# Kernel optimization log

Measured on AMD Instinct MI355X. Metric: run time of the kernel, lower is better.

Reference implementation:

```python
import jax, jax.numpy as jnp
import numpy as np

N = 50000      # nodes
E = 600000     # edges (no self-loops in data; GATConv adds them)
IN = 128       # input_dim
HID = 16       # hidden_dim
H1 = 8         # heads1
H2 = 4         # heads2
OUT = 40       # output_dim (classes)
EPS_BN = 1e-5
NEG_SLOPE = 0.2


def setup_inputs() -> dict:
    key = jax.random.key(0)
    ks = jax.random.split(key, 40)
    f32 = jnp.float32

    def p(k, shape, scale=0.1):
        return (jax.random.normal(k, shape) * scale).astype(f32)

    x = jax.random.normal(ks[0], (N, IN), f32)
    src = jax.random.randint(ks[1], (E,), 0, N)
    off = jax.random.randint(ks[2], (E,), 1, N)
    dst = (src + off) % N  # guarantees src != dst
    edge_index = jnp.stack([src, dst]).astype(jnp.int32)

    D1 = HID * H1  # 128
    D2 = HID * H2  # 64
    inp = {
        "x": x, "edge_index": edge_index,
        # conv1: IN -> HID per head, H1 heads, concat
        "W1": p(ks[3], (IN, H1 * HID)), "as1": p(ks[4], (H1, HID)), "ad1": p(ks[5], (H1, HID)), "b1": p(ks[6], (D1,)),
        "g1": jnp.ones((D1,), f32), "be1": jnp.zeros((D1,), f32),
        # conv_mid: D1 -> D1, 1 head, mean (concat=False)
        "Wm": p(ks[7], (D1, D1)), "asm": p(ks[8], (1, D1)), "adm": p(ks[9], (1, D1)), "bm": p(ks[10], (D1,)),
        "gm": jnp.ones((D1,), f32), "bem": jnp.zeros((D1,), f32),
        # conv2: D1 -> HID per head, H2 heads, concat
        "W2": p(ks[11], (D1, H2 * HID)), "as2": p(ks[12], (H2, HID)), "ad2": p(ks[13], (H2, HID)), "b2": p(ks[14], (D2,)),
        "g2": jnp.ones((D2,), f32), "be2": jnp.zeros((D2,), f32),
        # conv3: D2 -> OUT, 1 head, mean
        "W3": p(ks[15], (D2, OUT)), "as3": p(ks[16], (1, OUT)), "ad3": p(ks[17], (1, OUT)), "b3": p(ks[18], (OUT,)),
        "g3": jnp.ones((OUT,), f32), "be3": jnp.zeros((OUT,), f32),
    }
    return inp


def _gat(x, src, dst, W, a_s, a_d, b, concat):
    """PyG GATConv forward (self-loops already appended to src/dst)."""
    Nn = x.shape[0]
    H, C = a_s.shape
    h = (x @ W).reshape(Nn, H, C)                       # [N,H,C]
    s = (h * a_s).sum(-1)                               # [N,H] source score
    d = (h * a_d).sum(-1)                               # [N,H] dest score
    e = jax.nn.leaky_relu(s[src] + d[dst], NEG_SLOPE)   # [E,H]
    # segment softmax over incoming edges of each dst node
    m = jax.ops.segment_max(e, dst, num_segments=Nn)    # [N,H]
    ee = jnp.exp(e - m[dst])
    den = jax.ops.segment_sum(ee, dst, num_segments=Nn)
    alpha = ee / (den[dst] + 1e-16)                     # [E,H]
    out = jax.ops.segment_sum(h[src] * alpha[:, :, None], dst, num_segments=Nn)  # [N,H,C]
    out = out.reshape(Nn, H * C) if concat else out.mean(axis=1)
    return out + b


def _bn(x, g, b):
    mu = x.mean(axis=0)
    var = x.var(axis=0)
    return g * (x - mu) * jax.lax.rsqrt(var + EPS_BN) + b


def reference(x, edge_index, W1, as1, ad1, b1, g1, be1, Wm, asm, adm, bm, gm, bem,
              W2, as2, ad2, b2, g2, be2, W3, as3, ad3, b3, g3, be3):
    Nn = x.shape[0]
    loops = jnp.arange(Nn, dtype=edge_index.dtype)
    src = jnp.concatenate([edge_index[0], loops])
    dst = jnp.concatenate([edge_index[1], loops])

    h = jax.nn.elu(_bn(_gat(x, src, dst, W1, as1, ad1, b1, True), g1, be1))
    res = h
    h = jax.nn.elu(_bn(_gat(h, src, dst, Wm, asm, adm, bm, False), gm, bem))
    h = res + h
    h = jax.nn.elu(_bn(_gat(h, src, dst, W2, as2, ad2, b2, True), g2, be2))
    h = _bn(_gat(h, src, dst, W3, as3, ad3, b3, False), g3, be3)
    return jax.nn.log_softmax(h, axis=1)
```

## Files before the change

### kernel.cpp

```cpp
#include <hip/hip_runtime.h>
#include <hip/hip_bf16.h>
#include <math.h>

#define NN 50000
#define NE 600000
#define ET (NN + NE)

typedef __hip_bfloat16 bf16;
typedef __attribute__((ext_vector_type(8))) short bf16x8;
typedef __attribute__((ext_vector_type(4))) float f32x4;

static __device__ inline unsigned short f2bf(float f) {
    union { __hip_bfloat16 h; unsigned short u; } v;
    v.h = __float2bfloat16(f);
    return v.u;
}
static __device__ inline float bf2f(bf16 h) { return __bfloat162float(h); }

__global__ void k_hist(const int* __restrict__ ei, int* __restrict__ deg) {
    int e = blockIdx.x * blockDim.x + threadIdx.x;
    if (e >= ET) return;
    int d = (e < NE) ? ei[NE + e] : (e - NE);
    atomicAdd(&deg[d], 1);
}

__global__ void k_scan_local(const int* __restrict__ deg, int* __restrict__ tmp,
                             int* __restrict__ csum) {
    __shared__ int wsum[16];
    int i = blockIdx.x * 1024 + threadIdx.x;
    int lane = threadIdx.x & 63, wid = threadIdx.x >> 6;
    int x = (i < NN) ? deg[i] : 0;
    for (int off = 1; off < 64; off <<= 1) {
        int y = __shfl_up(x, off);
        if (lane >= off) x += y;
    }
    if (lane == 63) wsum[wid] = x;
    __syncthreads();
    if (wid == 0) {
        int t = (lane < 16) ? wsum[lane] : 0;
        for (int off = 1; off < 16; off <<= 1) {
            int y = __shfl_up(t, off);
            if (lane >= off) t += y;
        }
        if (lane < 16) wsum[lane] = t;
    }
    __syncthreads();
    if (wid > 0) x += wsum[wid - 1];
    if (i < NN) tmp[i] = x;
    if (threadIdx.x == 1023) csum[blockIdx.x] = x;
}

__global__ void k_scan_chunks(int* __restrict__ csum, int nchunks) {
    int lane = threadIdx.x;
    int v = (lane < nchunks) ? csum[lane] : 0;
    for (int off = 1; off < 64; off <<= 1) {
        int y = __shfl_up(v, off);
        if (lane >= off) v += y;
    }
    if (lane < nchunks) csum[lane] = v;
}

__global__ void k_rowptr(const int* __restrict__ tmp, const int* __restrict__ csum,
                         int* __restrict__ rowptr) {
    int i = blockIdx.x * blockDim.x + threadIdx.x;
    if (i == 0) rowptr[0] = 0;
    if (i < NN) {
        int chunk = i >> 10;
        int off = (chunk > 0) ? csum[chunk - 1] : 0;
        rowptr[i + 1] = tmp[i] + off;
    }
}

__global__ void k_fill(const int* __restrict__ ei, const int* __restrict__ rowptr,
                       int* __restrict__ fill, int* __restrict__ csr) {
    int e = blockIdx.x * blockDim.x + threadIdx.x;
    if (e >= ET) return;
    int s = (e < NE) ? ei[e] : (e - NE);
    int d = (e < NE) ? ei[NE + e] : (e - NE);
    int pos = atomicAdd(&fill[d], 1);
    csr[rowptr[d] + pos] = s;
}

__global__ void k_wconv_all(const float* __restrict__ W1, const float* __restrict__ Wm,
                            const float* __restrict__ W2, short* __restrict__ WT1,
                            short* __restrict__ WTm, short* __restrict__ WT2) {
    int idx = blockIdx.x * 256 + threadIdx.x;
    if (idx < 16384) {
        int d = idx >> 7, k = idx & 127;
        WT1[idx] = (short)f2bf(W1[k * 128 + d]);
    } else if (idx < 32768) {
        int i2 = idx - 16384;
        int d = i2 >> 7, k = i2 & 127;
        WTm[i2] = (short)f2bf(Wm[k * 128 + d]);
    } else if (idx < 40960) {
        int i3 = idx - 32768;
        int d = i3 >> 7, k = i3 & 127;
        WT2[i3] = (short)f2bf(W2[k * 64 + d]);
    }
}

template <int D>
__global__ void k_bnfin(const float* __restrict__ sums, const float* __restrict__ g,
                        const float* __restrict__ be, float2* __restrict__ ss) {
    int c = threadIdx.x;
    if (c >= D) return;
    float mu = sums[c] * (1.f / NN);
    float var = sums[128 + c] * (1.f / NN) - mu * mu;
    float sc = g[c] * rsqrtf(var + 1e-5f);
    ss[c] = make_float2(sc, be[c] - mu * sc);
}

template <int D, int HF, int MODE>
__global__ __launch_bounds__(64) void k_gemm_mfma(const float* __restrict__ Xf,
                                                  const bf16* __restrict__ X1,
                                                  const float2* __restrict__ ss1,
                                                  const bf16* __restrict__ X2,
                                                  const float2* __restrict__ ss2,
                                                  const short* __restrict__ WT,
                                                  bf16* __restrict__ Hout,
                                                  const float* __restrict__ a_s,
                                                  const float* __restrict__ a_d,
                                                  float* __restrict__ S,
                                                  float* __restrict__ Dv) {
    constexpr int K = 128;
    constexpr int NT = D / 16;
    int lane = threadIdx.x;
    int rb = blockIdx.x * 16;
    int m = lane & 15, kg = lane >> 4;

    f32x4 acc[NT];
#pragma unroll
    for (int n = 0; n < NT; n++) acc[n] = (f32x4){0.f, 0.f, 0.f, 0.f};

#pragma unroll
    for (int k0 = 0; k0 < K; k0 += 32) {
        int cb = k0 + kg * 8;
        bf16x8 a;
        if constexpr (MODE == 0) {
            const float* xp = Xf + (size_t)(rb + m) * K + cb;
            float4 f0 = *reinterpret_cast<const float4*>(xp);
            float4 f1 = *reinterpret_cast<const float4*>(xp + 4);
            a[0] = (short)f2bf(f0.x); a[1] = (short)f2bf(f0.y);
            a[2] = (short)f2bf(f0.z); a[3] = (short)f2bf(f0.w);
            a[4] = (short)f2bf(f1.x); a[5] = (short)f2bf(f1.y);
            a[6] = (short)f2bf(f1.z); a[7] = (short)f2bf(f1.w);
        } else {
            bf16x8 r1 = *reinterpret_cast<const bf16x8*>(X1 + (size_t)(rb + m) * K + cb);
            bf16x8 r2;
            if constexpr (MODE == 2)
                r2 = *reinterpret_cast<const bf16x8*>(X2 + (size_t)(rb + m) * K + cb);
#pragma unroll
            for (int j = 0; j < 8; j++) {
                float2 p1 = ss1[cb + j];
                bf16 b1; *(short*)&b1 = r1[j];
                float v = p1.x * bf2f(b1) + p1.y;
                v = (v > 0.f) ? v : (__expf(v) - 1.f);
                if constexpr (MODE == 2) {
                    float2 p2 = ss2[cb + j];
                    bf16 b2; *(short*)&b2 = r2[j];
                    float v2 = p2.x * bf2f(b2) + p2.y;
                    v2 = (v2 > 0.f) ? v2 : (__expf(v2) - 1.f);
                    v += v2;
                }
                a[j] = (short)f2bf(v);
            }
        }
#pragma unroll
        for (int n = 0; n < NT; n++) {
            bf16x8 b = *reinterpret_cast<const bf16x8*>(WT + (size_t)(n * 16 + m) * K + cb);
            acc[n] = __builtin_amdgcn_mfma_f32_16x16x32_bf16(a, b, acc[n], 0, 0, 0);
        }
    }

    float asv[NT], adv[NT];
#pragma unroll
    for (int n = 0; n < NT; n++) {
        asv[n] = a_s[n * 16 + m];
        adv[n] = a_d[n * 16 + m];
    }
#pragma unroll
    for (int r = 0; r < 4; r++) {
        int row = rb + kg * 4 + r;
#pragma unroll
        for (int n = 0; n < NT; n++)
            Hout[(size_t)row * D + n * 16 + m] = __float2bfloat16(acc[n][r]);
        if constexpr (HF == 1) {
            float sa = 0.f, da = 0.f;
#pragma unroll
            for (int n = 0; n < NT; n++) {
                sa += acc[n][r] * asv[n];
                da += acc[n][r] * adv[n];
            }
            for (int off = 1; off < 16; off <<= 1) {
                sa += __shfl_xor(sa, off);
                da += __shfl_xor(da, off);
            }
            if (m == 0) { S[row] = sa; Dv[row] = da; }
        } else {
#pragma unroll
            for (int n = 0; n < NT; n++) {
                float sa = acc[n][r] * asv[n];
                float da = acc[n][r] * adv[n];
                for (int off = 1; off < 16; off <<= 1) {
                    sa += __shfl_xor(sa, off);
                    da += __shfl_xor(da, off);
                }
                if (m == 0) { S[row * HF + n] = sa; Dv[row * HF + n] = da; }
            }
        }
    }
}

__global__ void k_gemm_small(const bf16* __restrict__ X, const float2* __restrict__ ss,
                             const float* __restrict__ W, bf16* __restrict__ Hout,
                             const float* __restrict__ a_s, const float* __restrict__ a_d,
                             float* __restrict__ S, float* __restrict__ Dv) {
    __shared__ float xs[64];
    int n = blockIdx.x, t = threadIdx.x;
    {
        float2 p = ss[t];
        float v = p.x * bf2f(X[n * 64 + t]) + p.y;
        xs[t] = (v > 0.f) ? v : (__expf(v) - 1.f);
    }
    __syncthreads();
    float acc = 0.f;
    if (t < 40) {
#pragma unroll
        for (int k = 0; k < 64; k++) acc += xs[k] * W[k * 40 + t];
        Hout[n * 40 + t] = __float2bfloat16(acc);
    }
    float sa = (t < 40) ? acc * a_s[t] : 0.f;
    float da = (t < 40) ? acc * a_d[t] : 0.f;
    for (int off = 32; off; off >>= 1) {
        sa += __shfl_xor(sa, off);
        da += __shfl_xor(da, off);
    }
    if (t == 0) {
        S[n] = sa;
        Dv[n] = da;
    }
}

template <int H, int C, int D>
__global__ __launch_bounds__(256) void k_aggregate(const bf16* __restrict__ Hb,
                                                   const float* __restrict__ S,
                                                   const float* __restrict__ Dv,
                                                   const int* __restrict__ rowptr,
                                                   const int* __restrict__ csr,
                                                   bf16* __restrict__ Out) {
    constexpr int WCAP = 64;
    __shared__ float wl[4][WCAP * H];
    int nl = threadIdx.x >> 6;
    int node = blockIdx.x * 4 + nl;
    if (node >= NN) return;
    int lane = threadIdx.x & 63;
    int r0 = rowptr[node], r1 = rowptr[node + 1];
    int cnt = r1 - r0;
    float dn[H], den[H];
#pragma unroll
    for (int h = 0; h < H; h++) {
        dn[h] = Dv[node * H + h];
        den[h] = 0.f;
    }
    for (int k = lane; k < cnt; k += 64) {
        int u = csr[r0 + k];
        float sv[H];
        if constexpr (H == 8) {
            float4 s0 = *reinterpret_cast<const float4*>(S + (size_t)u * 8);
            float4 s1 = *reinterpret_cast<const float4*>(S + (size_t)u * 8 + 4);
            sv[0] = s0.x; sv[1] = s0.y; sv[2] = s0.z; sv[3] = s0.w;
            sv[4] = s1.x; sv[5] = s1.y; sv[6] = s1.z; sv[7] = s1.w;
        } else if constexpr (H == 4) {
            float4 s0 = *reinterpret_cast<const float4*>(S + (size_t)u * 4);
            sv[0] = s0.x; sv[1] = s0.y; sv[2] = s0.z; sv[3] = s0.w;
        } else {
            sv[0] = S[u];
        }
        float ex[H];
#pragma unroll
        for (int h = 0; h < H; h++) {
            float e = sv[h] + dn[h];
            e = fmaxf(e, 0.2f * e);
            ex[h] = __expf(e);
            den[h] += ex[h];
        }
        if (k < WCAP) {
#pragma unroll
            for (int h = 0; h < H; h++) wl[nl][k * H + h] = ex[h];
        }
    }
#pragma unroll
    for (int h = 0; h < H; h++) {
        for (int off = 32; off; off >>= 1) den[h] += __shfl_xor(den[h], off);
        den[h] = 1.f / (den[h] + 1e-16f);
    }

    constexpr int EPI = (D > 64) ? 1 : 2;
    constexpr int LP = 64 / EPI;
    int sub = lane / LP;
    int j = lane % LP;
    bool act = (2 * j) < D;
    const int h_l = act ? (2 * j) / C : 0;
    float dninv_l = den[0], dn_l = dn[0];
#pragma unroll
    for (int h = 1; h < H; h++) {
        dninv_l = (h_l == h) ? den[h] : dninv_l;
        dn_l = (h_l == h) ? dn[h] : dn_l;
    }
    const float* wlp = &wl[nl][0];
    auto wof = [&](int idx, int u) -> float {
        if (idx < WCAP) return wlp[idx * H + h_l];
        float e = S[(size_t)u * H + h_l] + dn_l;
        e = fmaxf(e, 0.2f * e);
        return __expf(e);
    };
    float ax = 0.f, ay = 0.f;
    int k = sub;
    for (; k + 3 * EPI < cnt; k += 4 * EPI) {
        int u0 = csr[r0 + k];
        int u1 = csr[r0 + k + EPI];
        int u2 = csr[r0 + k + 2 * EPI];
        int u3 = csr[r0 + k + 3 * EPI];
        unsigned p0 = 0, p1 = 0, p2 = 0, p3 = 0;
        if (act) {
            p0 = *reinterpret_cast<const unsigned*>(Hb + (size_t)u0 * D + 2 * j);
            p1 = *reinterpret_cast<const unsigned*>(Hb + (size_t)u1 * D + 2 * j);
            p2 = *reinterpret_cast<const unsigned*>(Hb + (size_t)u2 * D + 2 * j);
            p3 = *reinterpret_cast<const unsigned*>(Hb + (size_t)u3 * D + 2 * j);
        }
        float w0 = wof(k, u0), w1 = wof(k + EPI, u1);
        float w2 = wof(k + 2 * EPI, u2), w3 = wof(k + 3 * EPI, u3);
        ax += w0 * __uint_as_float(p0 << 16) + w1 * __uint_as_float(p1 << 16) +
              w2 * __uint_as_float(p2 << 16) + w3 * __uint_as_float(p3 << 16);
        ay += w0 * __uint_as_float(p0 & 0xffff0000u) + w1 * __uint_as_float(p1 & 0xffff0000u) +
              w2 * __uint_as_float(p2 & 0xffff0000u) + w3 * __uint_as_float(p3 & 0xffff0000u);
    }
    for (; k < cnt; k += EPI) {
        int u = csr[r0 + k];
        unsigned pv = 0;
        if (act) pv = *reinterpret_cast<const unsigned*>(Hb + (size_t)u * D + 2 * j);
        float w = wof(k, u);
        ax += w * __uint_as_float(pv << 16);
        ay += w * __uint_as_float(pv & 0xffff0000u);
    }
    if (EPI == 2) {
        ax += __shfl_xor(ax, 32);
        ay += __shfl_xor(ay, 32);
    }
    if (act && lane < LP) {
        unsigned o = (unsigned)f2bf(ax * dninv_l) | ((unsigned)f2bf(ay * dninv_l) << 16);
        *reinterpret_cast<unsigned*>(Out + (size_t)node * D + 2 * j) = o;
    }
}

template <int D>
__global__ void k_bnstats(const bf16* __restrict__ X, float* __restrict__ sums) {
    int col = threadIdx.x;
    if (col >= D) return;
    float s = 0.f, q = 0.f;
    for (int r = blockIdx.x; r < NN; r += gridDim.x) {
        float v = bf2f(X[(size_t)r * D + col]);
        s += v;
        q += v * v;
    }
    atomicAdd(&sums[col], s);
    atomicAdd(&sums[128 + col], q);
}

__global__ void k_bn_logsoftmax(const bf16* __restrict__ X, const float* __restrict__ sums,
                                const float* __restrict__ g, const float* __restrict__ be,
                                float* __restrict__ Out) {
    int node = (blockIdx.x * blockDim.x + threadIdx.x) >> 6;
    int lane = threadIdx.x & 63;
    if (node >= NN) return;
    float bnv = 0.f, v = -1e30f;
    if (lane < 40) {
        float mu = sums[lane] * (1.f / NN);
        float var = sums[128 + lane] * (1.f / NN) - mu * mu;
        float sc = g[lane] * rsqrtf(var + 1e-5f);
        bnv = sc * (bf2f(X[node * 40 + lane]) - mu) + be[lane];
        v = bnv;
    }
    float m = v;
    for (int off = 32; off; off >>= 1) m = fmaxf(m, __shfl_xor(m, off));
    float ex = (lane < 40) ? expf(bnv - m) : 0.f;
    for (int off = 32; off; off >>= 1) ex += __shfl_xor(ex, off);
    float lse = m + logf(ex);
    if (lane < 40) Out[node * 40 + lane] = bnv - lse;
}

extern "C" void kernel_launch(void* const* d_in, const int* in_sizes, int n_in,
                              void* d_out, int out_size, void* d_ws, size_t ws_size,
                              hipStream_t stream) {
    (void)in_sizes; (void)n_in; (void)out_size; (void)ws_size;
    const float* x   = (const float*)d_in[0];
    const int*   ei  = (const int*)d_in[1];
    const float* W1  = (const float*)d_in[2];
    const float* as1 = (const float*)d_in[3];
    const float* ad1 = (const float*)d_in[4];
    const float* g1  = (const float*)d_in[6];
    const float* be1 = (const float*)d_in[7];
    const float* Wm  = (const float*)d_in[8];
    const float* asm_ = (const float*)d_in[9];
    const float* adm = (const float*)d_in[10];
    const float* gm  = (const float*)d_in[12];
    const float* bem = (const float*)d_in[13];
    const float* W2  = (const float*)d_in[14];
    const float* as2 = (const float*)d_in[15];
    const float* ad2 = (const float*)d_in[16];
    const float* g2  = (const float*)d_in[18];
    const float* be2 = (const float*)d_in[19];
    const float* W3  = (const float*)d_in[20];
    const float* as3 = (const float*)d_in[21];
    const float* ad3 = (const float*)d_in[22];
    const float* g3  = (const float*)d_in[24];
    const float* be3 = (const float*)d_in[25];
    float* out = (float*)d_out;

    char* ws = (char*)d_ws;
    size_t off = 0;
    auto alloc = [&](size_t b) {
        void* p = ws + off;
        off = (off + b + 255) & ~(size_t)255;
        return p;
    };
    int* rowptr = (int*)alloc((NN + 1) * 4);
    int* csr    = (int*)alloc((size_t)ET * 4);
    int* deg    = (int*)alloc(NN * 4);
    int* tmp    = (int*)alloc(NN * 4);
    int* csum   = (int*)alloc(256 * 4);
    bf16* Hbf   = (bf16*)alloc((size_t)NN * 128 * 2);
    bf16* AG1   = (bf16*)alloc((size_t)NN * 128 * 2);
    bf16* AG2   = (bf16*)alloc((size_t)NN * 128 * 2);
    bf16* AG3   = (bf16*)alloc((size_t)NN * 64 * 2);
    bf16* AG4   = (bf16*)alloc((size_t)NN * 40 * 2);
    float* S    = (float*)alloc((size_t)NN * 8 * 4);
    float* Dv   = (float*)alloc((size_t)NN * 8 * 4);
    float* bns  = (float*)alloc(4 * 256 * 4);
    float2* ss1 = (float2*)alloc(128 * 8);
    float2* ssM = (float2*)alloc(128 * 8);
    float2* ss2 = (float2*)alloc(64 * 8);
    short* WT1  = (short*)alloc(128 * 128 * 2);
    short* WTm  = (short*)alloc(128 * 128 * 2);
    short* WT2  = (short*)alloc(128 * 64 * 2);

    const int nchunks = (NN + 1023) / 1024;

    hipMemsetAsync(bns, 0, 4 * 256 * 4, stream);
    k_wconv_all<<<160, 256, 0, stream>>>(W1, Wm, W2, WT1, WTm, WT2);

    hipMemsetAsync(deg, 0, NN * 4, stream);
    k_hist<<<(ET + 255) / 256, 256, 0, stream>>>(ei, deg);
    k_scan_local<<<nchunks, 1024, 0, stream>>>(deg, tmp, csum);
    k_scan_chunks<<<1, 64, 0, stream>>>(csum, nchunks);
    k_rowptr<<<(NN + 255) / 256, 256, 0, stream>>>(tmp, csum, rowptr);
    hipMemsetAsync(deg, 0, NN * 4, stream);
    k_fill<<<(ET + 255) / 256, 256, 0, stream>>>(ei, rowptr, deg, csr);

    const int mfma_blocks = NN / 16;
    const int node_wave_blocks = (NN + 3) / 4;

    k_gemm_mfma<128, 8, 0><<<mfma_blocks, 64, 0, stream>>>(x, nullptr, nullptr, nullptr, nullptr,
                                                           WT1, Hbf, as1, ad1, S, Dv);
    k_aggregate<8, 16, 128><<<node_wave_blocks, 256, 0, stream>>>(Hbf, S, Dv, rowptr, csr, AG1);
    k_bnstats<128><<<512, 128, 0, stream>>>(AG1, bns + 0 * 256);
    k_bnfin<128><<<1, 128, 0, stream>>>(bns + 0 * 256, g1, be1, ss1);

    k_gemm_mfma<128, 1, 1><<<mfma_blocks, 64, 0, stream>>>(nullptr, AG1, ss1, nullptr, nullptr,
                                                           WTm, Hbf, asm_, adm, S, Dv);
    k_aggregate<1, 128, 128><<<node_wave_blocks, 256, 0, stream>>>(Hbf, S, Dv, rowptr, csr, AG2);
    k_bnstats<128><<<512, 128, 0, stream>>>(AG2, bns + 1 * 256);
    k_bnfin<128><<<1, 128, 0, stream>>>(bns + 1 * 256, gm, bem, ssM);

    k_gemm_mfma<64, 4, 2><<<mfma_blocks, 64, 0, stream>>>(nullptr, AG2, ssM, AG1, ss1,
                                                          WT2, Hbf, as2, ad2, S, Dv);
    k_aggregate<4, 16, 64><<<node_wave_blocks, 256, 0, stream>>>(Hbf, S, Dv, rowptr, csr, AG3);
    k_bnstats<64><<<512, 64, 0, stream>>>(AG3, bns + 2 * 256);
    k_bnfin<64><<<1, 64, 0, stream>>>(bns + 2 * 256, g2, be2, ss2);

    k_gemm_small<<<NN, 64, 0, stream>>>(AG3, ss2, W3, Hbf, as3, ad3, S, Dv);
    k_aggregate<1, 40, 40><<<node_wave_blocks, 256, 0, stream>>>(Hbf, S, Dv, rowptr, csr, AG4);
    k_bnstats<40><<<512, 64, 0, stream>>>(AG4, bns + 3 * 256);
    k_bn_logsoftmax<<<node_wave_blocks, 256, 0, stream>>>(AG4, bns + 3 * 256, g3, be3, out);
}
```

Before: 581.0 us.

## Fuse setup kernels, merge BN finalize into stats, simplify aggregate softmax

Merges the histogram with the weight conversion, the chunk scan with rowptr, and the CSR fill with the first-layer GEMM into single launches. BN finalize is folded into the stats kernel through a last-block counter. The three memsets become one. The aggregate kernel drops its separate denominator pass and LDS weight cache and computes the softmax denominator inline with the weighted sum, using batched loads. Together these cut launch count and a pass over edge scores, at the cost of recomputing exp per lane group and adding atomic and fence overhead in the BN finalize.

New measurement: 565.1 us. 2.7% less time.

```diff
diff --git a/kernel.cpp b/kernel.cpp
--- a/kernel.cpp
+++ b/kernel.cpp
@@ -5,6 +5,9 @@
 #define NN 50000
 #define NE 600000
 #define ET (NN + NE)
+#define FILLB ((ET + 255) / 256)
+#define NTILE (NN / 16)
+#define GEMMB ((NTILE + 3) / 4)
 
 typedef __hip_bfloat16 bf16;
 typedef __attribute__((ext_vector_type(8))) short bf16x8;
@@ -17,11 +20,32 @@
 }
 static __device__ inline float bf2f(bf16 h) { return __bfloat162float(h); }
 
-__global__ void k_hist(const int* __restrict__ ei, int* __restrict__ deg) {
-    int e = blockIdx.x * blockDim.x + threadIdx.x;
-    if (e >= ET) return;
-    int d = (e < NE) ? ei[NE + e] : (e - NE);
-    atomicAdd(&deg[d], 1);
+__global__ void k_hist_wconv(const int* __restrict__ ei, int* __restrict__ deg,
+                             const float* __restrict__ W1, const float* __restrict__ Wm,
+                             const float* __restrict__ W2, short* __restrict__ WT1,
+                             short* __restrict__ WTm, short* __restrict__ WT2) {
+    int b = blockIdx.x;
+    if (b < FILLB) {
+        int e = b * 256 + threadIdx.x;
+        if (e < ET) {
+            int d = (e < NE) ? ei[NE + e] : (e - NE);
+            atomicAdd(&deg[d], 1);
+        }
+    } else {
+        int idx = (b - FILLB) * 256 + threadIdx.x;
+        if (idx < 16384) {
+            int d = idx >> 7, k = idx & 127;
+            WT1[idx] = (short)f2bf(W1[k * 128 + d]);
+        } else if (idx < 32768) {
+            int i2 = idx - 16384;
+            int d = i2 >> 7, k = i2 & 127;
+            WTm[i2] = (short)f2bf(Wm[k * 128 + d]);
+        } else if (idx < 40960) {
+            int i3 = idx - 32768;
+            int d = i3 >> 7, k = i3 & 127;
+            WT2[i3] = (short)f2bf(W2[k * 64 + d]);
+        }
+    }
 }
 
 __global__ void k_scan_local(const int* __restrict__ deg, int* __restrict__ tmp,
@@ -50,82 +74,38 @@
     if (threadIdx.x == 1023) csum[blockIdx.x] = x;
 }
 
-__global__ void k_scan_chunks(int* __restrict__ csum, int nchunks) {
-    int lane = threadIdx.x;
-    int v = (lane < nchunks) ? csum[lane] : 0;
-    for (int off = 1; off < 64; off <<= 1) {
-        int y = __shfl_up(v, off);
-        if (lane >= off) v += y;
-    }
-    if (lane < nchunks) csum[lane] = v;
-}
-
 __global__ void k_rowptr(const int* __restrict__ tmp, const int* __restrict__ csum,
-                         int* __restrict__ rowptr) {
+                         int* __restrict__ rowptr, int nchunks) {
+    __shared__ int pref[64];
+    if (threadIdx.x < 64) {
+        int lane = threadIdx.x;
+        int v = (lane < nchunks) ? csum[lane] : 0;
+        for (int off = 1; off < 64; off <<= 1) {
+            int y = __shfl_up(v, off);
+            if (lane >= off) v += y;
+        }
+        pref[lane] = v;
+    }
+    __syncthreads();
     int i = blockIdx.x * blockDim.x + threadIdx.x;
     if (i == 0) rowptr[0] = 0;
     if (i < NN) {
         int chunk = i >> 10;
-        int off = (chunk > 0) ? csum[chunk - 1] : 0;
+        int off = (chunk > 0) ? pref[chunk - 1] : 0;
         rowptr[i + 1] = tmp[i] + off;
     }
 }
 
-__global__ void k_fill(const int* __restrict__ ei, const int* __restrict__ rowptr,
-                       int* __restrict__ fill, int* __restrict__ csr) {
-    int e = blockIdx.x * blockDim.x + threadIdx.x;
-    if (e >= ET) return;
-    int s = (e < NE) ? ei[e] : (e - NE);
-    int d = (e < NE) ? ei[NE + e] : (e - NE);
-    int pos = atomicAdd(&fill[d], 1);
-    csr[rowptr[d] + pos] = s;
-}
-
-__global__ void k_wconv_all(const float* __restrict__ W1, const float* __restrict__ Wm,
-                            const float* __restrict__ W2, short* __restrict__ WT1,
-                            short* __restrict__ WTm, short* __restrict__ WT2) {
-    int idx = blockIdx.x * 256 + threadIdx.x;
-    if (idx < 16384) {
-        int d = idx >> 7, k = idx & 127;
-        WT1[idx] = (short)f2bf(W1[k * 128 + d]);
-    } else if (idx < 32768) {
-        int i2 = idx - 16384;
-        int d = i2 >> 7, k = i2 & 127;
-        WTm[i2] = (short)f2bf(Wm[k * 128 + d]);
-    } else if (idx < 40960) {
-        int i3 = idx - 32768;
-        int d = i3 >> 7, k = i3 & 127;
-        WT2[i3] = (short)f2bf(W2[k * 64 + d]);
-    }
-}
-
-template <int D>
-__global__ void k_bnfin(const float* __restrict__ sums, const float* __restrict__ g,
-                        const float* __restrict__ be, float2* __restrict__ ss) {
-    int c = threadIdx.x;
-    if (c >= D) return;
-    float mu = sums[c] * (1.f / NN);
-    float var = sums[128 + c] * (1.f / NN) - mu * mu;
-    float sc = g[c] * rsqrtf(var + 1e-5f);
-    ss[c] = make_float2(sc, be[c] - mu * sc);
-}
-
 template <int D, int HF, int MODE>
-__global__ __launch_bounds__(64) void k_gemm_mfma(const float* __restrict__ Xf,
-                                                  const bf16* __restrict__ X1,
-                                                  const float2* __restrict__ ss1,
-                                                  const bf16* __restrict__ X2,
-                                                  const float2* __restrict__ ss2,
-                                                  const short* __restrict__ WT,
-                                                  bf16* __restrict__ Hout,
-                                                  const float* __restrict__ a_s,
-                                                  const float* __restrict__ a_d,
-                                                  float* __restrict__ S,
-                                                  float* __restrict__ Dv) {
+static __device__ __forceinline__ void gemm_body(int tile, int lane,
+    const float* __restrict__ Xf, const bf16* __restrict__ X1, const float2* __restrict__ ss1,
+    const bf16* __restrict__ X2, const float2* __restrict__ ss2,
+    const short* __restrict__ WT, bf16* __restrict__ Hout,
+    const float* __restrict__ a_s, const float* __restrict__ a_d,
+    float* __restrict__ S, float* __restrict__ Dv) {
     constexpr int K = 128;
     constexpr int NT = D / 16;
-    int lane = threadIdx.x;
-    int rb = blockIdx.x * 16;
+    int rb = tile * 16;
     int m = lane & 15, kg = lane >> 4;
 
     f32x4 acc[NT];
@@ -211,6 +191,39 @@
     }
 }
 
+template <int D, int HF, int MODE>
+__global__ __launch_bounds__(64) void k_gemm_mfma(const float* Xf, const bf16* X1,
+                                                  const float2* ss1, const bf16* X2,
+                                                  const float2* ss2, const short* WT,
+                                                  bf16* Hout, const float* a_s,
+                                                  const float* a_d, float* S, float* Dv) {
+    gemm_body<D, HF, MODE>(blockIdx.x, threadIdx.x, Xf, X1, ss1, X2, ss2, WT, Hout, a_s, a_d, S, Dv);
+}
+
+__global__ __launch_bounds__(256) void k_fill_gemm1(const int* __restrict__ ei,
+                                                    const int* __restrict__ rowptr,
+                                                    int* __restrict__ fill, int* __restrict__ csr,
+                                                    const float* __restrict__ x,
+                                                    const short* __restrict__ WT1,
+                                                    bf16* __restrict__ Hout,
+                                                    const float* __restrict__ as1,
+                                                    const float* __restrict__ ad1,
+                                                    float* __restrict__ S, float* __restrict__ Dv) {
+    if (blockIdx.x < FILLB) {
+        int e = blockIdx.x * 256 + threadIdx.x;
+        if (e >= ET) return;
+        int s = (e < NE) ? ei[e] : (e - NE);
+        int d = (e < NE) ? ei[NE + e] : (e - NE);
+        int pos = atomicAdd(&fill[d], 1);
+        csr[rowptr[d] + pos] = s;
+        return;
+    }
+    int tile = (blockIdx.x - FILLB) * 4 + (threadIdx.x >> 6);
+    if (tile >= NTILE) return;
+    gemm_body<128, 8, 0>(tile, threadIdx.x & 63, x, nullptr, nullptr, nullptr, nullptr,
+                         WT1, Hout, as1, ad1, S, Dv);
+}
+
 __global__ void k_gemm_small(const bf16* __restrict__ X, const float2* __restrict__ ss,
                              const float* __restrict__ W, bf16* __restrict__ Hout,
                              const float* __restrict__ a_s, const float* __restrict__ a_d,
@@ -248,123 +261,95 @@
                                                    const int* __restrict__ rowptr,
                                                    const int* __restrict__ csr,
                                                    bf16* __restrict__ Out) {
-    constexpr int WCAP = 64;
-    __shared__ float wl[4][WCAP * H];
-    int nl = threadIdx.x >> 6;
-    int node = blockIdx.x * 4 + nl;
+    int node = blockIdx.x * 4 + (threadIdx.x >> 6);
     if (node >= NN) return;
     int lane = threadIdx.x & 63;
     int r0 = rowptr[node], r1 = rowptr[node + 1];
     int cnt = r1 - r0;
-    float dn[H], den[H];
-#pragma unroll
-    for (int h = 0; h < H; h++) {
-        dn[h] = Dv[node * H + h];
-        den[h] = 0.f;
-    }
-    for (int k = lane; k < cnt; k += 64) {
-        int u = csr[r0 + k];
-        float sv[H];
-        if constexpr (H == 8) {
-            float4 s0 = *reinterpret_cast<const float4*>(S + (size_t)u * 8);
-            float4 s1 = *reinterpret_cast<const float4*>(S + (size_t)u * 8 + 4);
-            sv[0] = s0.x; sv[1] = s0.y; sv[2] = s0.z; sv[3] = s0.w;
-            sv[4] = s1.x; sv[5] = s1.y; sv[6] = s1.z; sv[7] = s1.w;
-        } else if constexpr (H == 4) {
-            float4 s0 = *reinterpret_cast<const float4*>(S + (size_t)u * 4);
-            sv[0] = s0.x; sv[1] = s0.y; sv[2] = s0.z; sv[3] = s0.w;
-        } else {
-            sv[0] = S[u];
-        }
-        float ex[H];
-#pragma unroll
-        for (int h = 0; h < H; h++) {
-            float e = sv[h] + dn[h];
-            e = fmaxf(e, 0.2f * e);
-            ex[h] = __expf(e);
-            den[h] += ex[h];
-        }
-        if (k < WCAP) {
-#pragma unroll
-            for (int h = 0; h < H; h++) wl[nl][k * H + h] = ex[h];
-        }
-    }
-#pragma unroll
-    for (int h = 0; h < H; h++) {
-        for (int off = 32; off; off >>= 1) den[h] += __shfl_xor(den[h], off);
-        den[h] = 1.f / (den[h] + 1e-16f);
-    }
-
     constexpr int EPI = (D > 64) ? 1 : 2;
     constexpr int LP = 64 / EPI;
     int sub = lane / LP;
     int j = lane % LP;
     bool act = (2 * j) < D;
     const int h_l = act ? (2 * j) / C : 0;
-    float dninv_l = den[0], dn_l = dn[0];
-#pragma unroll
-    for (int h = 1; h < H; h++) {
-        dninv_l = (h_l == h) ? den[h] : dninv_l;
-        dn_l = (h_l == h) ? dn[h] : dn_l;
-    }
-    const float* wlp = &wl[nl][0];
-    auto wof = [&](int idx, int u) -> float {
-        if (idx < WCAP) return wlp[idx * H + h_l];
+    float dn_l = Dv[node * H + h_l];
+
+    float ax = 0.f, ay = 0.f, den = 0.f;
+    int k = sub;
+    for (; k + 3 * EPI < cnt; k += 4 * EPI) {
+        int uu[4];
+        float svv[4];
+        unsigned pp[4];
+#pragma unroll
+        for (int i = 0; i < 4; i++) uu[i] = csr[r0 + k + i * EPI];
+#pragma unroll
+        for (int i = 0; i < 4; i++) svv[i] = S[(size_t)uu[i] * H + h_l];
+#pragma unroll
+        for (int i = 0; i < 4; i++)
+            pp[i] = act ? *reinterpret_cast<const unsigned*>(Hb + (size_t)uu[i] * D + 2 * j) : 0u;
+#pragma unroll
+        for (int i = 0; i < 4; i++) {
+            float e = svv[i] + dn_l;
+            e = fmaxf(e, 0.2f * e);
+            float w = __expf(e);
+            den += w;
+            ax += w * __uint_as_float(pp[i] << 16);
+            ay += w * __uint_as_float(pp[i] & 0xffff0000u);
+        }
+    }
+    for (; k < cnt; k += EPI) {
+        int u = csr[r0 + k];
         float e = S[(size_t)u * H + h_l] + dn_l;
         e = fmaxf(e, 0.2f * e);
-        return __expf(e);
-    };
-    float ax = 0.f, ay = 0.f;
-    int k = sub;
-    for (; k + 3 * EPI < cnt; k += 4 * EPI) {
-        int u0 = csr[r0 + k];
-        int u1 = csr[r0 + k + EPI];
-        int u2 = csr[r0 + k + 2 * EPI];
-        int u3 = csr[r0 + k + 3 * EPI];
-        unsigned p0 = 0, p1 = 0, p2 = 0, p3 = 0;
-        if (act) {
-            p0 = *reinterpret_cast<const unsigned*>(Hb + (size_t)u0 * D + 2 * j);
-            p1 = *reinterpret_cast<const unsigned*>(Hb + (size_t)u1 * D + 2 * j);
-            p2 = *reinterpret_cast<const unsigned*>(Hb + (size_t)u2 * D + 2 * j);
-            p3 = *reinterpret_cast<const unsigned*>(Hb + (size_t)u3 * D + 2 * j);
-        }
-        float w0 = wof(k, u0), w1 = wof(k + EPI, u1);
-        float w2 = wof(k + 2 * EPI, u2), w3 = wof(k + 3 * EPI, u3);
-        ax += w0 * __uint_as_float(p0 << 16) + w1 * __uint_as_float(p1 << 16) +
-              w2 * __uint_as_float(p2 << 16) + w3 * __uint_as_float(p3 << 16);
-        ay += w0 * __uint_as_float(p0 & 0xffff0000u) + w1 * __uint_as_float(p1 & 0xffff0000u) +
-              w2 * __uint_as_float(p2 & 0xffff0000u) + w3 * __uint_as_float(p3 & 0xffff0000u);
-    }
-    for (; k < cnt; k += EPI) {
-        int u = csr[r0 + k];
-        unsigned pv = 0;
-        if (act) pv = *reinterpret_cast<const unsigned*>(Hb + (size_t)u * D + 2 * j);
-        float w = wof(k, u);
+        float w = __expf(e);
+        den += w;
+        unsigned pv = act ? *reinterpret_cast<const unsigned*>(Hb + (size_t)u * D + 2 * j) : 0u;
         ax += w * __uint_as_float(pv << 16);
         ay += w * __uint_as_float(pv & 0xffff0000u);
     }
     if (EPI == 2) {
         ax += __shfl_xor(ax, 32);
         ay += __shfl_xor(ay, 32);
+        den += __shfl_xor(den, 32);
     }
     if (act && lane < LP) {
-        unsigned o = (unsigned)f2bf(ax * dninv_l) | ((unsigned)f2bf(ay * dninv_l) << 16);
+        float inv = 1.f / (den + 1e-16f);
+        unsigned o = (unsigned)f2bf(ax * inv) | ((unsigned)f2bf(ay * inv) << 16);
         *reinterpret_cast<unsigned*>(Out + (size_t)node * D + 2 * j) = o;
     }
 }
 
-template <int D>
-__global__ void k_bnstats(const bf16* __restrict__ X, float* __restrict__ sums) {
+template <int D, bool FIN>
+__global__ void k_bnstats(const bf16* __restrict__ X, float* __restrict__ sums,
+                          int* __restrict__ cnt, const float* __restrict__ g,
+                          const float* __restrict__ be, float2* __restrict__ ss) {
     int col = threadIdx.x;
-    if (col >= D) return;
-    float s = 0.f, q = 0.f;
-    for (int r = blockIdx.x; r < NN; r += gridDim.x) {
-        float v = bf2f(X[(size_t)r * D + col]);
-        s += v;
-        q += v * v;
-    }
-    atomicAdd(&sums[col], s);
-    atomicAdd(&sums[128 + col], q);
+    if (col < D) {
+        float s = 0.f, q = 0.f;
+        for (int r = blockIdx.x; r < NN; r += gridDim.x) {
+            float v = bf2f(X[(size_t)r * D + col]);
+            s += v;
+            q += v * v;
+        }
+        atomicAdd(&sums[col], s);
+        atomicAdd(&sums[128 + col], q);
+    }
+    if constexpr (FIN) {
+        __shared__ int lastFlag;
+        __threadfence();
+        __syncthreads();
+        if (threadIdx.x == 0)
+            lastFlag = (atomicAdd(cnt, 1) == (int)gridDim.x - 1) ? 1 : 0;
+        __syncthreads();
+        if (lastFlag && col < D) {
+            float su = atomicAdd(&sums[col], 0.f);
+            float sq = atomicAdd(&sums[128 + col], 0.f);
+            float mu = su * (1.f / NN);
+            float var = sq * (1.f / NN) - mu * mu;
+            float sc = g[col] * rsqrtf(var + 1e-5f);
+            ss[col] = make_float2(sc, be[col] - mu * sc);
+        }
+    }
 }
 
 __global__ void k_bn_logsoftmax(const bf16* __restrict__ X, const float* __restrict__ sums,
@@ -426,7 +411,12 @@
     };
     int* rowptr = (int*)alloc((NN + 1) * 4);
     int* csr    = (int*)alloc((size_t)ET * 4);
-    int* deg    = (int*)alloc(NN * 4);
+    const size_t ZB = (size_t)NN * 4 + (size_t)NN * 4 + 1024 * 4 + 16;
+    char* zb    = (char*)alloc(ZB);
+    int* deg    = (int*)zb;
+    int* fillc  = (int*)(zb + (size_t)NN * 4);
+    float* bns  = (float*)(zb + 2 * (size_t)NN * 4);
+    int* cnt    = (int*)(zb + 2 * (size_t)NN * 4 + 1024 * 4);
     int* tmp    = (int*)alloc(NN * 4);
     int* csum   = (int*)alloc(256 * 4);
     bf16* Hbf   = (bf16*)alloc((size_t)NN * 128 * 2);
@@ -436,7 +426,6 @@
     bf16* AG4   = (bf16*)alloc((size_t)NN * 40 * 2);
     float* S    = (float*)alloc((size_t)NN * 8 * 4);
     float* Dv   = (float*)alloc((size_t)NN * 8 * 4);
-    float* bns  = (float*)alloc(4 * 256 * 4);
     float2* ss1 = (float2*)alloc(128 * 8);
     float2* ssM = (float2*)alloc(128 * 8);
     float2* ss2 = (float2*)alloc(64 * 8);
@@ -445,41 +434,25 @@
     short* WT2  = (short*)alloc(128 * 64 * 2);
 
     const int nchunks = (NN + 1023) / 1024;
-
-    hipMemsetAsync(bns, 0, 4 * 256 * 4, stream);
-    k_wconv_all<<<160, 256, 0, stream>>>(W1, Wm, W2, WT1, WTm, WT2);
-
-    hipMemsetAsync(deg, 0, NN * 4, stream);
-    k_hist<<<(ET + 255) / 256, 256, 0, stream>>>(ei, deg);
+    const int node_wave_blocks = (NN + 3) / 4;
+
+    hipMemsetAsync(zb, 0, ZB, stream);
+    k_hist_wconv<<<FILLB + 160, 256, 0, stream>>>(ei, deg, W1, Wm, W2, WT1, WTm, WT2);
     k_scan_local<<<nchunks, 1024, 0, stream>>>(deg, tmp, csum);
-    k_scan_chunks<<<1, 64, 0, stream>>>(csum, nchunks);
-    k_rowptr<<<(NN + 255) / 256, 256, 0, stream>>>(tmp, csum, rowptr);
-    hipMemsetAsync(deg, 0, NN * 4, stream);
-    k_fill<<<(ET + 255) / 256, 256, 0, stream>>>(ei, rowptr, deg, csr);
-
-    const int mfma_blocks = NN / 16;
-    const int node_wave_blocks = (NN + 3) / 4;
-
-    k_gemm_mfma<128, 8, 0><<<mfma_blocks, 64, 0, stream>>>(x, nullptr, nullptr, nullptr, nullptr,
-                                                           WT1, Hbf, as1, ad1, S, Dv);
+    k_rowptr<<<(NN + 255) / 256, 256, 0, stream>>>(tmp, csum, rowptr, nchunks);
+    k_fill_gemm1<<<FILLB + GEMMB, 256, 0, stream>>>(ei, rowptr, fillc, csr, x, WT1, Hbf, as1, ad1, S, Dv);
     k_aggregate<8, 16, 128><<<node_wave_blocks, 256, 0, stream>>>(Hbf, S, Dv, rowptr, csr, AG1);
-    k_bnstats<128><<<512, 128, 0, stream>>>(AG1, bns + 0 * 256);
-    k_bnfin<128><<<1, 128, 0, stream>>>(bns + 0 * 256, g1, be1, ss1);
-
-    k_gemm_mfma<128, 1, 1><<<mfma_blocks, 64, 0, stream>>>(nullptr, AG1, ss1, nullptr, nullptr,
-                                                           WTm, Hbf, asm_, adm, S, Dv);
+    k_bnstats<128, true><<<512, 128, 0, stream>>>(AG1, bns + 0 * 256, cnt + 0, g1, be1, ss1);
+    k_gemm_mfma<128, 1, 1><<<NTILE, 64, 0, stream>>>(nullptr, AG1, ss1, nullptr, nullptr, WTm,
+                                                     Hbf, asm_, adm, S, Dv);
     k_aggregate<1, 128, 128><<<node_wave_blocks, 256, 0, stream>>>(Hbf, S, Dv, rowptr, csr, AG2);
-    k_bnstats<128><<<512, 128, 0, stream>>>(AG2, bns + 1 * 256);
-    k_bnfin<128><<<1, 128, 0, stream>>>(bns + 1 * 256, gm, bem, ssM);
-
-    k_gemm_mfma<64, 4, 2><<<mfma_blocks, 64, 0, stream>>>(nullptr, AG2, ssM, AG1, ss1,
-                                                          WT2, Hbf, as2, ad2, S, Dv);
+    k_bnstats<128, true><<<512, 128, 0, stream>>>(AG2, bns + 1 * 256, cnt + 1, gm, bem, ssM);
+    k_gemm_mfma<64, 4, 2><<<NTILE, 64, 0, stream>>>(nullptr, AG2, ssM, AG1, ss1, WT2,
+                                                    Hbf, as2, ad2, S, Dv);
     k_aggregate<4, 16, 64><<<node_wave_blocks, 256, 0, stream>>>(Hbf, S, Dv, rowptr, csr, AG3);
-    k_bnstats<64><<<512, 64, 0, stream>>>(AG3, bns + 2 * 256);
-    k_bnfin<64><<<1, 64, 0, stream>>>(bns + 2 * 256, g2, be2, ss2);
-
+    k_bnstats<64, true><<<512, 64, 0, stream>>>(AG3, bns + 2 * 256, cnt + 2, g2, be2, ss2);
     k_gemm_small<<<NN, 64, 0, stream>>>(AG3, ss2, W3, Hbf, as3, ad3, S, Dv);
     k_aggregate<1, 40, 40><<<node_wave_blocks, 256, 0, stream>>>(Hbf, S, Dv, rowptr, csr, AG4);
-    k_bnstats<40><<<512, 64, 0, stream>>>(AG4, bns + 3 * 256);
+    k_bnstats<40, false><<<512, 64, 0, stream>>>(AG4, bns + 3 * 256, nullptr, nullptr, nullptr, nullptr);
     k_bn_logsoftmax<<<node_wave_blocks, 256, 0, stream>>>(AG4, bns + 3 * 256, g3, be3, out);
 }
```
